# Optimization experiments

Measured on AMD Instinct MI355X. Metric: run time of the kernel, lower is better.

The kernel has to match this reference:

```python
import jax, jax.numpy as jnp
import numpy as np

DIM = 1024
NUM_EXPERTS = 8
TOP_K = 2
HIDDEN = int(DIM * 4.0 * 2 / 3)  # 2730, matches GatedMLP hidden_dim
AUX_COEF = 0.01


def setup_inputs() -> dict:
    key = jax.random.key(0)
    ks = jax.random.split(key, 5)
    B, N = 4, 2048
    x = jax.random.normal(ks[0], (B, N, DIM), dtype=jnp.float32)
    # nn.Linear weights are [out, in]; y = x @ W.T
    gate_w = jax.random.normal(ks[1], (NUM_EXPERTS, DIM), dtype=jnp.float32) * 0.02
    w1 = jax.random.normal(ks[2], (NUM_EXPERTS, HIDDEN, DIM), dtype=jnp.float32) * 0.02
    w2 = jax.random.normal(ks[3], (NUM_EXPERTS, DIM, HIDDEN), dtype=jnp.float32) * 0.02
    w3 = jax.random.normal(ks[4], (NUM_EXPERTS, HIDDEN, DIM), dtype=jnp.float32) * 0.02
    return {"x": x, "gate_w": gate_w, "w1": w1, "w2": w2, "w3": w3}


def reference(x, gate_w, w1, w2, w3):
    # Router
    logits = jnp.einsum('bnd,ed->bne', x, gate_w)            # [B,N,E]
    probs = jax.nn.softmax(logits, axis=-1)                   # [B,N,E]
    top_v, top_i = jax.lax.top_k(probs, TOP_K)                # [B,N,K]
    top_v = top_v / jnp.sum(top_v, axis=-1, keepdims=True)
    # Combine weights per expert: sum_k prob_k * 1[idx_k == e]  -> [B,N,E]
    one_hot = jax.nn.one_hot(top_i, NUM_EXPERTS, dtype=x.dtype)  # [B,N,K,E]
    combine = jnp.einsum('bnk,bnke->bne', top_v, one_hot)
    # Per-expert SwiGLU MLP (dropout is identity in eval)
    out = jnp.zeros_like(x)
    for e in range(NUM_EXPERTS):
        h = jax.nn.silu(jnp.einsum('bnd,hd->bnh', x, w1[e])) \
            * jnp.einsum('bnd,hd->bnh', x, w3[e])             # [B,N,H]
        y = jnp.einsum('bnh,dh->bnd', h, w2[e])               # [B,N,D]
        out = out + combine[..., e:e + 1] * y
    # Load-balancing aux loss
    tokens_per_expert = jnp.mean(probs, axis=(0, 1))          # [E]
    uniform = 1.0 / NUM_EXPERTS
    aux_loss = AUX_COEF * jnp.mean((tokens_per_expert - uniform) ** 2)
    return out, aux_loss
```

## Files before the change

### kernel.cpp

```cpp
#include <hip/hip_runtime.h>
#include <hip/hip_bf16.h>
#include <stdint.h>

#define DIM   1024
#define NE    8
#define HID   2730
#define HPAD  2752
#define NTOK  8192
#define CAP   8192

typedef __bf16 bf16x8 __attribute__((ext_vector_type(8)));
typedef float  floatx4 __attribute__((ext_vector_type(4)));

__device__ __forceinline__ unsigned short f2bf(float f) {
    union { float f; unsigned int u; } v; v.f = f;
    unsigned int u = v.u;
    unsigned int r = (u + 0x7fffu + ((u >> 16) & 1u)) >> 16;
    return (unsigned short)r;
}

__device__ __forceinline__ void gl2lds16(const void* g, void* l) {
    __builtin_amdgcn_global_load_lds((const __attribute__((address_space(1))) void*)g,
                                     (__attribute__((address_space(3))) void*)l,
                                     16, 0, 0);
}

__global__ void convert_x_kernel(const float* __restrict__ x, unsigned short* __restrict__ xb) {
    int i = blockIdx.x * 256 + threadIdx.x;
    float4 v = ((const float4*)x)[i];
    uint2 o;
    o.x = (unsigned)f2bf(v.x) | ((unsigned)f2bf(v.y) << 16);
    o.y = (unsigned)f2bf(v.z) | ((unsigned)f2bf(v.w) << 16);
    *(uint2*)(xb + i * 4) = o;
}

__global__ void convert_w13_kernel(const float* __restrict__ w1, const float* __restrict__ w3,
                                   unsigned short* __restrict__ w1b, unsigned short* __restrict__ w3b) {
    const int HALF = (NE * HID * DIM) / 4;
    int i = blockIdx.x * 256 + threadIdx.x;
    const float* src; unsigned short* dst; int j;
    if (i < HALF) { src = w1; dst = w1b; j = i; }
    else          { src = w3; dst = w3b; j = i - HALF; }
    float4 v = ((const float4*)src)[j];
    uint2 o;
    o.x = (unsigned)f2bf(v.x) | ((unsigned)f2bf(v.y) << 16);
    o.y = (unsigned)f2bf(v.z) | ((unsigned)f2bf(v.w) << 16);
    *(uint2*)(dst + (size_t)j * 4) = o;
}

__global__ void convert_w2_kernel(const float* __restrict__ w2, unsigned short* __restrict__ w2b) {
    int i = blockIdx.x * 256 + threadIdx.x;
    int r = i / 688;
    int c = (i - r * 688) * 4;
    const float* src = w2 + r * HID;
    unsigned short q[4];
#pragma unroll
    for (int j = 0; j < 4; ++j) {
        int col = c + j;
        q[j] = (col < HID) ? f2bf(src[col]) : (unsigned short)0;
    }
    uint2 o;
    o.x = (unsigned)q[0] | ((unsigned)q[1] << 16);
    o.y = (unsigned)q[2] | ((unsigned)q[3] << 16);
    *(uint2*)(w2b + (size_t)r * HPAD + c) = o;
}

__global__ void router_kernel(const float* __restrict__ x, const float* __restrict__ gw,
                              int* __restrict__ toks, float* __restrict__ wts,
                              int* __restrict__ counts, float* __restrict__ psum) {
    __shared__ float gws[NE * DIM];
    __shared__ float pblk[4][NE];
    int t = threadIdx.x;
    for (int i = t; i < NE * DIM; i += 256) gws[i] = gw[i];
    __syncthreads();

    int wv = t >> 6, lane = t & 63;
    int tok = blockIdx.x * 4 + wv;
    const float4* x4 = (const float4*)(x + (size_t)tok * DIM);

    float p[NE];
#pragma unroll
    for (int e = 0; e < NE; ++e) p[e] = 0.f;
#pragma unroll
    for (int c = 0; c < 4; ++c) {
        float4 xv = x4[c * 64 + lane];
#pragma unroll
        for (int e = 0; e < NE; ++e) {
            float4 gv = ((const float4*)(gws + e * DIM))[c * 64 + lane];
            p[e] += xv.x * gv.x + xv.y * gv.y + xv.z * gv.z + xv.w * gv.w;
        }
    }
#pragma unroll
    for (int e = 0; e < NE; ++e)
#pragma unroll
        for (int s = 32; s; s >>= 1) p[e] += __shfl_xor(p[e], s, 64);

    if (lane == 0) {
        float mx = p[0];
#pragma unroll
        for (int e = 1; e < NE; ++e) mx = fmaxf(mx, p[e]);
        float ex[NE], s = 0.f;
#pragma unroll
        for (int e = 0; e < NE; ++e) { ex[e] = __expf(p[e] - mx); s += ex[e]; }
        float inv = 1.f / s;
        int i1 = 0, i2 = 0; float v1 = -1.f, v2 = -1.f;
#pragma unroll
        for (int e = 0; e < NE; ++e) {
            float pe = ex[e] * inv;
            pblk[wv][e] = pe;
            if (pe > v1)      { v2 = v1; i2 = i1; v1 = pe; i1 = e; }
            else if (pe > v2) { v2 = pe; i2 = e; }
        }
        float wn = 1.f / (v1 + v2);
        int p1 = atomicAdd(&counts[i1], 1);
        toks[i1 * CAP + p1] = tok; wts[i1 * CAP + p1] = v1 * wn;
        int p2 = atomicAdd(&counts[i2], 1);
        toks[i2 * CAP + p2] = tok; wts[i2 * CAP + p2] = v2 * wn;
    }
    __syncthreads();
    if (t < NE) {
        float s = pblk[0][t] + pblk[1][t] + pblk[2][t] + pblk[3][t];
        atomicAdd(&psum[t], s);
    }
}

__global__ void finalize_kernel(const int* __restrict__ counts, int* __restrict__ offs,
                                const float* __restrict__ psum, float* __restrict__ aux_out) {
    if (threadIdx.x == 0) {
        int off = 0;
        for (int e = 0; e < NE; ++e) { offs[e] = off; off += counts[e]; }
        float s = 0.f;
        for (int e = 0; e < NE; ++e) {
            float d = psum[e] * (1.f / NTOK) - (1.f / NE);
            s += d * d;
        }
        aux_out[0] = 0.01f * s * (1.f / NE);
    }
}

__global__ __launch_bounds__(256, 2) void gemm1_kernel(
    const unsigned short* __restrict__ xb,
    const unsigned short* __restrict__ w1b,
    const unsigned short* __restrict__ w3b,
    unsigned short* __restrict__ h,
    const int* __restrict__ counts, const int* __restrict__ offs,
    const int* __restrict__ toks) {
    const int e = blockIdx.z;
    const int M = counts[e];
    const int m0 = blockIdx.y * 128;
    if (m0 >= M) return;
    const int n0 = blockIdx.x * 128;

    __shared__ unsigned short As[128 * 64];
    __shared__ unsigned short B1s[128 * 64];
    __shared__ unsigned short B3s[128 * 64];

    const int t = threadIdx.x;
    const int rb = t >> 3;
    const int kc = (t & 7) * 8;
    const int* tl = toks + e * CAP;
    int arow[4], brow[4];
#pragma unroll
    for (int i = 0; i < 4; ++i) {
        arow[i] = tl[min(m0 + rb + i * 32, M - 1)];
        brow[i] = min(n0 + rb + i * 32, HID - 1);
    }
    const unsigned short* w1e = w1b + (size_t)e * HID * DIM;
    const unsigned short* w3e = w3b + (size_t)e * HID * DIM;

    floatx4 acc1[4][4], acc3[4][4];
#pragma unroll
    for (int a = 0; a < 4; ++a)
#pragma unroll
        for (int b = 0; b < 4; ++b) {
            acc1[a][b] = (floatx4){0.f, 0.f, 0.f, 0.f};
            acc3[a][b] = (floatx4){0.f, 0.f, 0.f, 0.f};
        }

    const int wv = t >> 6, lane = t & 63;
    const int wm = (wv & 1) * 64, wn = (wv >> 1) * 64;
    const int lr = lane & 15, lq = lane >> 4;

    for (int k0 = 0; k0 < DIM; k0 += 64) {
#pragma unroll
        for (int i = 0; i < 4; ++i) {
            const int ldso = (i * 256 + t) * 8;
            gl2lds16(xb + (size_t)arow[i] * DIM + k0 + kc, &As[ldso]);
            gl2lds16(w1e + (size_t)brow[i] * DIM + k0 + kc, &B1s[ldso]);
            gl2lds16(w3e + (size_t)brow[i] * DIM + k0 + kc, &B3s[ldso]);
        }
        __syncthreads();
#pragma unroll
        for (int kk = 0; kk < 64; kk += 32) {
            bf16x8 af[4];
#pragma unroll
            for (int mi = 0; mi < 4; ++mi)
                af[mi] = *(const bf16x8*)&As[(wm + mi * 16 + lr) * 64 + kk + lq * 8];
#pragma unroll
            for (int ni = 0; ni < 4; ++ni) {
                bf16x8 b1 = *(const bf16x8*)&B1s[(wn + ni * 16 + lr) * 64 + kk + lq * 8];
                bf16x8 b3 = *(const bf16x8*)&B3s[(wn + ni * 16 + lr) * 64 + kk + lq * 8];
#pragma unroll
                for (int mi = 0; mi < 4; ++mi) {
                    acc1[mi][ni] = __builtin_amdgcn_mfma_f32_16x16x32_bf16(af[mi], b1, acc1[mi][ni], 0, 0, 0);
                    acc3[mi][ni] = __builtin_amdgcn_mfma_f32_16x16x32_bf16(af[mi], b3, acc3[mi][ni], 0, 0, 0);
                }
            }
        }
        __syncthreads();
    }

    const int hb = offs[e];
#pragma unroll
    for (int mi = 0; mi < 4; ++mi) {
#pragma unroll
        for (int rg = 0; rg < 4; ++rg) {
            const int gm = m0 + wm + mi * 16 + lq * 4 + rg;
            if (gm >= M) continue;
            unsigned short* hrow = h + (size_t)(hb + gm) * HPAD;
#pragma unroll
            for (int ni = 0; ni < 4; ++ni) {
                const int col = n0 + wn + ni * 16 + lr;
                if (col >= HPAD) continue;
                float z1 = acc1[mi][ni][rg];
                float z3 = acc3[mi][ni][rg];
                float hv = z1 / (1.f + __expf(-z1)) * z3;
                hrow[col] = f2bf(hv);
            }
        }
    }
}

__global__ __launch_bounds__(256, 2) void gemm2_kernel(
    const unsigned short* __restrict__ h,
    const unsigned short* __restrict__ w2b,
    float* __restrict__ out,
    const int* __restrict__ counts, const int* __restrict__ offs,
    const int* __restrict__ toks, const float* __restrict__ wts) {
    const int e = blockIdx.z;
    const int M = counts[e];
    const int m0 = blockIdx.y * 128;
    if (m0 >= M) return;
    const int n0 = blockIdx.x * 128;

    __shared__ unsigned short As[128 * 64];
    __shared__ unsigned short Bs[128 * 64];

    const int t = threadIdx.x;
    const int rb = t >> 3;
    const int kc = (t & 7) * 8;
    const int hb = offs[e];
    int arow[4], brow[4];
#pragma unroll
    for (int i = 0; i < 4; ++i) {
        arow[i] = hb + min(m0 + rb + i * 32, M - 1);
        brow[i] = n0 + rb + i * 32;
    }
    const unsigned short* w2e = w2b + (size_t)e * DIM * HPAD;

    floatx4 acc[4][4];
#pragma unroll
    for (int a = 0; a < 4; ++a)
#pragma unroll
        for (int b = 0; b < 4; ++b) acc[a][b] = (floatx4){0.f, 0.f, 0.f, 0.f};

    const int wv = t >> 6, lane = t & 63;
    const int wm = (wv & 1) * 64, wn = (wv >> 1) * 64;
    const int lr = lane & 15, lq = lane >> 4;

    for (int k0 = 0; k0 < HPAD; k0 += 64) {
#pragma unroll
        for (int i = 0; i < 4; ++i) {
            const int ldso = (i * 256 + t) * 8;
            gl2lds16(h + (size_t)arow[i] * HPAD + k0 + kc, &As[ldso]);
            gl2lds16(w2e + (size_t)brow[i] * HPAD + k0 + kc, &Bs[ldso]);
        }
        __syncthreads();
#pragma unroll
        for (int kk = 0; kk < 64; kk += 32) {
            bf16x8 af[4];
#pragma unroll
            for (int mi = 0; mi < 4; ++mi)
                af[mi] = *(const bf16x8*)&As[(wm + mi * 16 + lr) * 64 + kk + lq * 8];
#pragma unroll
            for (int ni = 0; ni < 4; ++ni) {
                bf16x8 bf = *(const bf16x8*)&Bs[(wn + ni * 16 + lr) * 64 + kk + lq * 8];
#pragma unroll
                for (int mi = 0; mi < 4; ++mi)
                    acc[mi][ni] = __builtin_amdgcn_mfma_f32_16x16x32_bf16(af[mi], bf, acc[mi][ni], 0, 0, 0);
            }
        }
        __syncthreads();
    }

#pragma unroll
    for (int mi = 0; mi < 4; ++mi) {
#pragma unroll
        for (int rg = 0; rg < 4; ++rg) {
            const int gm = m0 + wm + mi * 16 + lq * 4 + rg;
            if (gm >= M) continue;
            const int sl = e * CAP + gm;
            const int tok = toks[sl];
            const float wt = wts[sl];
            float* orow = out + (size_t)tok * DIM;
#pragma unroll
            for (int ni = 0; ni < 4; ++ni) {
                const int col = n0 + wn + ni * 16 + lr;
                atomicAdd(&orow[col], wt * acc[mi][ni][rg]);
            }
        }
    }
}

extern "C" void kernel_launch(void* const* d_in, const int* in_sizes, int n_in,
                              void* d_out, int out_size, void* d_ws, size_t ws_size,
                              hipStream_t stream) {
    const float* x  = (const float*)d_in[0];
    const float* gw = (const float*)d_in[1];
    const float* w1 = (const float*)d_in[2];
    const float* w2 = (const float*)d_in[3];
    const float* w3 = (const float*)d_in[4];
    float* out = (float*)d_out;

    char* ws = (char*)d_ws;
    size_t o = 0;
    auto alloc = [&](size_t bytes) -> void* {
        void* p = ws + o;
        o += (bytes + 255) & ~(size_t)255;
        return p;
    };
    unsigned short* xb   = (unsigned short*)alloc((size_t)NTOK * DIM * 2);
    unsigned short* w1b  = (unsigned short*)alloc((size_t)NE * HID * DIM * 2);
    unsigned short* w3b  = (unsigned short*)alloc((size_t)NE * HID * DIM * 2);
    unsigned short* w2b  = (unsigned short*)alloc((size_t)NE * DIM * HPAD * 2);
    unsigned short* hbuf = (unsigned short*)alloc((size_t)2 * NTOK * HPAD * 2);
    int*   toks   = (int*)alloc((size_t)NE * CAP * 4);
    float* wts    = (float*)alloc((size_t)NE * CAP * 4);
    int*   counts = (int*)alloc(256);
    float* psum   = (float*)alloc(256);
    int*   offs   = (int*)alloc(256);
    if (o > ws_size) return;

    hipMemsetAsync(d_out, 0, (size_t)out_size * 4, stream);
    hipMemsetAsync(counts, 0, 256, stream);
    hipMemsetAsync(psum, 0, 256, stream);

    convert_x_kernel<<<8192, 256, 0, stream>>>(x, xb);
    convert_w13_kernel<<<43680, 256, 0, stream>>>(w1, w3, w1b, w3b);
    convert_w2_kernel<<<22016, 256, 0, stream>>>(w2, w2b);
    router_kernel<<<2048, 256, 0, stream>>>(x, gw, toks, wts, counts, psum);
    finalize_kernel<<<1, 64, 0, stream>>>(counts, offs, psum, out + (size_t)NTOK * DIM);
    gemm1_kernel<<<dim3(22, 64, 8), 256, 0, stream>>>(xb, w1b, w3b, hbuf, counts, offs, toks);
    gemm2_kernel<<<dim3(8, 64, 8), 256, 0, stream>>>(hbuf, w2b, out, counts, offs, toks, wts);
}
```

Measured before the change: 964.3 us.

## XOR-swizzle LDS tiles in both GEMMs and replace atomic scatter with combine kernel

```diff
diff --git a/kernel.cpp b/kernel.cpp
--- a/kernel.cpp
+++ b/kernel.cpp
@@ -66,7 +66,8 @@
 }
 
 __global__ void router_kernel(const float* __restrict__ x, const float* __restrict__ gw,
-                              int* __restrict__ toks, float* __restrict__ wts,
+                              int* __restrict__ toks, int* __restrict__ meta,
+                              float* __restrict__ tokw,
                               int* __restrict__ counts, float* __restrict__ psum) {
     __shared__ float gws[NE * DIM];
     __shared__ float pblk[4][NE];
@@ -113,9 +114,13 @@
         }
         float wn = 1.f / (v1 + v2);
         int p1 = atomicAdd(&counts[i1], 1);
-        toks[i1 * CAP + p1] = tok; wts[i1 * CAP + p1] = v1 * wn;
+        toks[i1 * CAP + p1] = tok;
+        meta[tok * 2]     = (i1 << 16) | p1;
+        tokw[tok * 2]     = v1 * wn;
         int p2 = atomicAdd(&counts[i2], 1);
-        toks[i2 * CAP + p2] = tok; wts[i2 * CAP + p2] = v2 * wn;
+        toks[i2 * CAP + p2] = tok;
+        meta[tok * 2 + 1] = (i2 << 16) | p2;
+        tokw[tok * 2 + 1] = v2 * wn;
     }
     __syncthreads();
     if (t < NE) {
@@ -157,7 +162,7 @@
 
     const int t = threadIdx.x;
     const int rb = t >> 3;
-    const int kc = (t & 7) * 8;
+    const int kc = ((t & 7) ^ (rb & 7)) * 8;
     const int* tl = toks + e * CAP;
     int arow[4], brow[4];
 #pragma unroll
@@ -180,6 +185,7 @@
     const int wv = t >> 6, lane = t & 63;
     const int wm = (wv & 1) * 64, wn = (wv >> 1) * 64;
     const int lr = lane & 15, lq = lane >> 4;
+    const int sw = lane & 7;
 
     for (int k0 = 0; k0 < DIM; k0 += 64) {
 #pragma unroll
@@ -192,14 +198,15 @@
         __syncthreads();
 #pragma unroll
         for (int kk = 0; kk < 64; kk += 32) {
+            const int pc = (((kk >> 3) + lq) ^ sw) * 8;
             bf16x8 af[4];
 #pragma unroll
             for (int mi = 0; mi < 4; ++mi)
-                af[mi] = *(const bf16x8*)&As[(wm + mi * 16 + lr) * 64 + kk + lq * 8];
+                af[mi] = *(const bf16x8*)&As[(wm + mi * 16 + lr) * 64 + pc];
 #pragma unroll
             for (int ni = 0; ni < 4; ++ni) {
-                bf16x8 b1 = *(const bf16x8*)&B1s[(wn + ni * 16 + lr) * 64 + kk + lq * 8];
-                bf16x8 b3 = *(const bf16x8*)&B3s[(wn + ni * 16 + lr) * 64 + kk + lq * 8];
+                bf16x8 b1 = *(const bf16x8*)&B1s[(wn + ni * 16 + lr) * 64 + pc];
+                bf16x8 b3 = *(const bf16x8*)&B3s[(wn + ni * 16 + lr) * 64 + pc];
 #pragma unroll
                 for (int mi = 0; mi < 4; ++mi) {
                     acc1[mi][ni] = __builtin_amdgcn_mfma_f32_16x16x32_bf16(af[mi], b1, acc1[mi][ni], 0, 0, 0);
@@ -234,9 +241,8 @@
 __global__ __launch_bounds__(256, 2) void gemm2_kernel(
     const unsigned short* __restrict__ h,
     const unsigned short* __restrict__ w2b,
-    float* __restrict__ out,
-    const int* __restrict__ counts, const int* __restrict__ offs,
-    const int* __restrict__ toks, const float* __restrict__ wts) {
+    float* __restrict__ y,
+    const int* __restrict__ counts, const int* __restrict__ offs) {
     const int e = blockIdx.z;
     const int M = counts[e];
     const int m0 = blockIdx.y * 128;
@@ -248,7 +254,7 @@
 
     const int t = threadIdx.x;
     const int rb = t >> 3;
-    const int kc = (t & 7) * 8;
+    const int kc = ((t & 7) ^ (rb & 7)) * 8;
     const int hb = offs[e];
     int arow[4], brow[4];
 #pragma unroll
@@ -267,6 +273,7 @@
     const int wv = t >> 6, lane = t & 63;
     const int wm = (wv & 1) * 64, wn = (wv >> 1) * 64;
     const int lr = lane & 15, lq = lane >> 4;
+    const int sw = lane & 7;
 
     for (int k0 = 0; k0 < HPAD; k0 += 64) {
 #pragma unroll
@@ -278,13 +285,14 @@
         __syncthreads();
 #pragma unroll
         for (int kk = 0; kk < 64; kk += 32) {
+            const int pc = (((kk >> 3) + lq) ^ sw) * 8;
             bf16x8 af[4];
 #pragma unroll
             for (int mi = 0; mi < 4; ++mi)
-                af[mi] = *(const bf16x8*)&As[(wm + mi * 16 + lr) * 64 + kk + lq * 8];
+                af[mi] = *(const bf16x8*)&As[(wm + mi * 16 + lr) * 64 + pc];
 #pragma unroll
             for (int ni = 0; ni < 4; ++ni) {
-                bf16x8 bf = *(const bf16x8*)&Bs[(wn + ni * 16 + lr) * 64 + kk + lq * 8];
+                bf16x8 bf = *(const bf16x8*)&Bs[(wn + ni * 16 + lr) * 64 + pc];
 #pragma unroll
                 for (int mi = 0; mi < 4; ++mi)
                     acc[mi][ni] = __builtin_amdgcn_mfma_f32_16x16x32_bf16(af[mi], bf, acc[mi][ni], 0, 0, 0);
@@ -299,17 +307,35 @@
         for (int rg = 0; rg < 4; ++rg) {
             const int gm = m0 + wm + mi * 16 + lq * 4 + rg;
             if (gm >= M) continue;
-            const int sl = e * CAP + gm;
-            const int tok = toks[sl];
-            const float wt = wts[sl];
-            float* orow = out + (size_t)tok * DIM;
+            float* yrow = y + (size_t)(hb + gm) * DIM;
 #pragma unroll
             for (int ni = 0; ni < 4; ++ni) {
                 const int col = n0 + wn + ni * 16 + lr;
-                atomicAdd(&orow[col], wt * acc[mi][ni][rg]);
+                yrow[col] = acc[mi][ni][rg];
             }
         }
     }
+}
+
+__global__ void combine_kernel(const float* __restrict__ y,
+                               const int* __restrict__ meta,
+                               const float* __restrict__ tokw,
+                               const int* __restrict__ offs,
+                               float* __restrict__ out) {
+    const int tok = blockIdx.x;
+    const int t = threadIdx.x;
+    const int m0 = meta[tok * 2], m1 = meta[tok * 2 + 1];
+    const float w0 = tokw[tok * 2], w1 = tokw[tok * 2 + 1];
+    const int r0 = offs[m0 >> 16] + (m0 & 0xffff);
+    const int r1 = offs[m1 >> 16] + (m1 & 0xffff);
+    float4 a = ((const float4*)(y + (size_t)r0 * DIM))[t];
+    float4 b = ((const float4*)(y + (size_t)r1 * DIM))[t];
+    float4 o;
+    o.x = w0 * a.x + w1 * b.x;
+    o.y = w0 * a.y + w1 * b.y;
+    o.z = w0 * a.z + w1 * b.z;
+    o.w = w0 * a.w + w1 * b.w;
+    ((float4*)(out + (size_t)tok * DIM))[t] = o;
 }
 
 extern "C" void kernel_launch(void* const* d_in, const int* in_sizes, int n_in,
@@ -335,21 +361,23 @@
     unsigned short* w2b  = (unsigned short*)alloc((size_t)NE * DIM * HPAD * 2);
     unsigned short* hbuf = (unsigned short*)alloc((size_t)2 * NTOK * HPAD * 2);
     int*   toks   = (int*)alloc((size_t)NE * CAP * 4);
-    float* wts    = (float*)alloc((size_t)NE * CAP * 4);
+    int*   meta   = (int*)alloc((size_t)NTOK * 2 * 4);
+    float* tokw   = (float*)alloc((size_t)NTOK * 2 * 4);
     int*   counts = (int*)alloc(256);
     float* psum   = (float*)alloc(256);
     int*   offs   = (int*)alloc(256);
     if (o > ws_size) return;
-
-    hipMemsetAsync(d_out, 0, (size_t)out_size * 4, stream);
+    float* ybuf = (float*)w1b;
+
     hipMemsetAsync(counts, 0, 256, stream);
     hipMemsetAsync(psum, 0, 256, stream);
 
     convert_x_kernel<<<8192, 256, 0, stream>>>(x, xb);
     convert_w13_kernel<<<43680, 256, 0, stream>>>(w1, w3, w1b, w3b);
     convert_w2_kernel<<<22016, 256, 0, stream>>>(w2, w2b);
-    router_kernel<<<2048, 256, 0, stream>>>(x, gw, toks, wts, counts, psum);
+    router_kernel<<<2048, 256, 0, stream>>>(x, gw, toks, meta, tokw, counts, psum);
     finalize_kernel<<<1, 64, 0, stream>>>(counts, offs, psum, out + (size_t)NTOK * DIM);
     gemm1_kernel<<<dim3(22, 64, 8), 256, 0, stream>>>(xb, w1b, w3b, hbuf, counts, offs, toks);
-    gemm2_kernel<<<dim3(8, 64, 8), 256, 0, stream>>>(hbuf, w2b, out, counts, offs, toks, wts);
-}
+    gemm2_kernel<<<dim3(8, 64, 8), 256, 0, stream>>>(hbuf, w2b, ybuf, counts, offs);
+    combine_kernel<<<NTOK, 256, 0, stream>>>(ybuf, meta, tokw, offs, out);
+}
```

After: 899.6 us. -6.7%, faster.
